# Kernel optimization log

Hardware: AMD Instinct MI355X
Metric: run time of the kernel (lower is better)

## Reference

```python
import jax, jax.numpy as jnp
import numpy as np

VAR_N, LEVELS, NCELLS, PRED_N = 4, 17, 56, 12
D = VAR_N * LEVELS          # 68
FLAT = VAR_N * D            # 272 = ntiles * interm in CrossConnector
T = 4096
DT = 0.1                    # fused-ODE solver step of the LTC cell


def _var_encoder(x, w1, b1, w2, b2, w3, b3, w4, b4, w5, b5):
    # nn.Sequential(Linear, ReLU, Linear, ReLU, Linear, ReLU, Linear, ReLU, Linear)
    h = jax.nn.relu(x @ w1 + b1)
    h = jax.nn.relu(h @ w2 + b2)
    h = jax.nn.relu(h @ w3 + b3)
    h = jax.nn.relu(h @ w4 + b4)
    return h @ w5 + b5


def _run_ltc(seq, wx, wh, b, a, tau, wout, bout):
    def cell(h, u):
        f = jax.nn.sigmoid(u @ wx + h @ wh + b)           # gated synaptic activation
        return (h + DT * f * a) / (1.0 + DT * (1.0 / (tau + 0.5) + f))

    def step_obs(h, u):
        h2 = cell(h, u)
        return h2, h2 @ wout + bout

    hT, vs1 = jax.lax.scan(step_obs, jnp.zeros((NCELLS,), seq.dtype), seq)

    def step_pred(carry, _):
        h, v = carry
        h2 = cell(h, v)
        v2 = h2 @ wout + bout
        return (h2, v2), v2

    _, vs2 = jax.lax.scan(step_pred, (hT, vs1[-1]), None, length=PRED_N)
    return jnp.concatenate([vs1, vs2], axis=0)        # (T+PRED_N, LEVELS)


def setup_inputs() -> dict:
    key = jax.random.key(0)
    ks = iter(jax.random.split(key, 64))
    d = {"x": jax.random.normal(next(ks), (T, D), jnp.float32)}

    def add_ve(prefix, inp, out):
        dims = [(inp, inp), (inp, inp), (inp, out), (out, out), (out, out)]
        for i, (fi, fo) in enumerate(dims, 1):
            d[f"{prefix}w{i}"] = jax.random.normal(next(ks), (fi, fo), jnp.float32) / np.sqrt(fi)
            d[f"{prefix}b{i}"] = jax.random.normal(next(ks), (fo,), jnp.float32) * 0.01

    add_ve("p", D, D)          # preproc  VarEncoder(68,68)
    add_ve("c1", LEVELS, D)    # CrossConnector inner VarEncoder(17,68)
    add_ve("c2", FLAT, D)      # CrossConnector outer VarEncoder(272,68)

    d["ltc_wx"] = jax.random.normal(next(ks), (VAR_N, LEVELS, NCELLS), jnp.float32) / np.sqrt(LEVELS)
    d["ltc_wh"] = jax.random.normal(next(ks), (VAR_N, NCELLS, NCELLS), jnp.float32) / np.sqrt(NCELLS)
    d["ltc_b"] = jax.random.normal(next(ks), (VAR_N, NCELLS), jnp.float32) * 0.01
    d["ltc_a"] = jax.random.normal(next(ks), (VAR_N, NCELLS), jnp.float32)
    d["ltc_tau"] = jax.random.uniform(next(ks), (VAR_N, NCELLS), jnp.float32)
    d["ltc_wout"] = jax.random.normal(next(ks), (VAR_N, NCELLS, LEVELS), jnp.float32) / np.sqrt(NCELLS)
    d["ltc_bout"] = jax.random.normal(next(ks), (VAR_N, LEVELS), jnp.float32) * 0.01
    return d


def reference(x, pw1, pb1, pw2, pb2, pw3, pb3, pw4, pb4, pw5, pb5,
              c1w1, c1b1, c1w2, c1b2, c1w3, c1b3, c1w4, c1b4, c1w5, c1b5,
              c2w1, c2b1, c2w2, c2b2, c2w3, c2b3, c2w4, c2b4, c2w5, c2b5,
              ltc_wx, ltc_wh, ltc_b, ltc_a, ltc_tau, ltc_wout, ltc_bout):
    pre = _var_encoder(x, pw1, pb1, pw2, pb2, pw3, pb3, pw4, pb4, pw5, pb5)   # (T, 68)
    xs = pre.reshape(VAR_N, -1, LEVELS)                                       # (4, T, 17) row-major, as torch.reshape
    vs = jax.vmap(_run_ltc)(xs, ltc_wx, ltc_wh, ltc_b, ltc_a, ltc_tau,
                            ltc_wout, ltc_bout)                               # (4, T+12, 17)
    vs = jnp.transpose(vs, (1, 0, 2))                                         # (T+12, 4, 17)
    y = jax.nn.relu(_var_encoder(vs, c1w1, c1b1, c1w2, c1b2, c1w3, c1b3,
                                 c1w4, c1b4, c1w5, c1b5))                     # (T+12, 4, 68)
    y = y.reshape(y.shape[0], -1)                                             # (T+12, 272)
    return _var_encoder(y, c2w1, c2b1, c2w2, c2b2, c2w3, c2b3,
                        c2w4, c2b4, c2w5, c2b5)                               # (T+12, 68)
```

## Files before the change

kernel.cpp:

```cpp
#include <hip/hip_runtime.h>
#include <hip/hip_bf16.h>
#include <math.h>

#define VAR_N 4
#define LEVELS 17
#define NCELLS 56
#define PRED_N 12
#define TSTEPS 4096
#define TROWS (TSTEPS + PRED_N)
#define DT 0.1f
#define RPB 8
#define LOG2E 1.44269504088896340736f
#define TB 8

static __device__ __forceinline__ float rl(float x, int lane) {
    return __int_as_float(__builtin_amdgcn_readlane(__float_as_int(x), lane));
}
static __device__ __forceinline__ float rcpf(float x) {
    return __builtin_amdgcn_rcpf(x);
}

__global__ void pre_g_kernel(const float* __restrict__ x,
                             const float* __restrict__ w1, const float* __restrict__ b1,
                             const float* __restrict__ w2, const float* __restrict__ b2,
                             const float* __restrict__ w3, const float* __restrict__ b3,
                             const float* __restrict__ w4, const float* __restrict__ b4,
                             const float* __restrict__ w5, const float* __restrict__ b5,
                             const float* __restrict__ wx, const float* __restrict__ bvec,
                             float* __restrict__ g) {
    __shared__ float lds[2 * RPB * 68];
    float* bufA = lds;
    float* bufB = lds + RPB * 68;
    const int r0 = blockIdx.x * RPB;
    const int tid = threadIdx.x;

    for (int idx = tid; idx < RPB * 68; idx += 256)
        bufA[idx] = x[(size_t)r0 * 68 + idx];
    __syncthreads();

    const float* Ws[5] = {w1, w2, w3, w4, w5};
    const float* Bs[5] = {b1, b2, b3, b4, b5};
    for (int L = 0; L < 5; ++L) {
        const float* __restrict__ W = Ws[L];
        const bool act = (L < 4);
        if (tid < 68) {
            const int j = tid;
            float acc[RPB];
            float bj = Bs[L][j];
#pragma unroll
            for (int r = 0; r < RPB; ++r) acc[r] = bj;
            for (int k = 0; k + 4 <= 68; k += 4) {
                float w0v = W[(k + 0) * 68 + j];
                float w1v = W[(k + 1) * 68 + j];
                float w2v = W[(k + 2) * 68 + j];
                float w3v = W[(k + 3) * 68 + j];
#pragma unroll
                for (int r = 0; r < RPB; ++r) {
                    const float4 hx = *(const float4*)(bufA + r * 68 + k);
                    acc[r] = fmaf(hx.x, w0v, fmaf(hx.y, w1v,
                              fmaf(hx.z, w2v, fmaf(hx.w, w3v, acc[r]))));
                }
            }
#pragma unroll
            for (int r = 0; r < RPB; ++r)
                bufB[r * 68 + j] = act ? fmaxf(acc[r], 0.f) : acc[r];
        }
        __syncthreads();
        float* t = bufA; bufA = bufB; bufB = t;
    }

    for (int idx = tid; idx < RPB * 4 * NCELLS; idx += 256) {
        int r = idx / 224;
        int rem = idx - r * 224;
        int q = rem / NCELLS;
        int j = rem - q * NCELLS;
        int gr = r0 + r;
        int v = gr >> 10;
        int trow = ((gr & 1023) << 2) + q;
        const float* arow = bufA + r * 68 + q * LEVELS;
        float acc = bvec[v * NCELLS + j];
#pragma unroll
        for (int l = 0; l < LEVELS; ++l)
            acc = fmaf(arow[l], wx[(v * LEVELS + l) * NCELLS + j], acc);
        g[((size_t)(v * NCELLS + j)) * TSTEPS + trow] = acc * LOG2E;
    }
}

__global__ void __launch_bounds__(64, 1) scan_kernel(
    const float* __restrict__ g, const float* __restrict__ wh,
    const float* __restrict__ a, const float* __restrict__ tau,
    const float* __restrict__ wx, const float* __restrict__ wout,
    const float* __restrict__ bout, const float* __restrict__ b,
    float* __restrict__ H) {
    typedef float v2 __attribute__((ext_vector_type(2)));
    const int v = blockIdx.x;
    const int lane = threadIdx.x;
    const bool active = lane < NCELLS;
    const int j = active ? lane : (NCELLS - 1);
    __shared__ __align__(16) float hbuf[64];

    v2 whp[28];
#pragma unroll
    for (int q = 0; q < 28; ++q) {
        float w0 = active ? wh[((size_t)v * NCELLS + 2 * q + 0) * NCELLS + lane] * LOG2E : 0.f;
        float w1 = active ? wh[((size_t)v * NCELLS + 2 * q + 1) * NCELLS + lane] * LOG2E : 0.f;
        v2 t; t.x = w0; t.y = w1;
        whp[q] = t;
    }
    const float alpha = active ? DT * a[v * NCELLS + lane] : 0.f;
    const float cden = active ? 1.f + DT / (tau[v * NCELLS + lane] + 0.5f) : 1.f;

    const float4* __restrict__ gv4 = (const float4*)(g + ((size_t)v * NCELLS + j) * TSTEPS);
    float* __restrict__ hp = H + (size_t)v * TROWS * NCELLS + lane;

    auto cell = [&](float h, float gcur) -> float {
        hbuf[lane] = h;
        const float4* h4 = (const float4*)hbuf;
        float4 hv[14];
#pragma unroll
        for (int q = 0; q < 14; ++q) hv[q] = h4[q];
        v2 a0 = {0.f, 0.f}, a1 = {0.f, 0.f}, a2 = {0.f, 0.f}, a3 = {0.f, 0.f};
#pragma unroll
        for (int q = 0; q < 7; ++q) {
            float4 hq0 = hv[2 * q];
            float4 hq1 = hv[2 * q + 1];
            v2 p0; p0.x = hq0.x; p0.y = hq0.y;
            v2 p1; p1.x = hq0.z; p1.y = hq0.w;
            v2 p2; p2.x = hq1.x; p2.y = hq1.y;
            v2 p3; p3.x = hq1.z; p3.y = hq1.w;
            a0 = __builtin_elementwise_fma(p0, whp[4 * q + 0], a0);
            a1 = __builtin_elementwise_fma(p1, whp[4 * q + 1], a1);
            a2 = __builtin_elementwise_fma(p2, whp[4 * q + 2], a2);
            a3 = __builtin_elementwise_fma(p3, whp[4 * q + 3], a3);
        }
        v2 s = (a0 + a1) + (a2 + a3);
        float z2 = (gcur + s.x) + s.y;
        float zc = fmaxf(z2, -80.f);
        float e = __builtin_amdgcn_exp2f(-zc);
        float t1 = 1.f + e;
        float num = fmaf(h, t1, alpha);
        float den = fmaf(cden, t1, DT);
        float hn = num * rcpf(den);
        __builtin_amdgcn_sched_group_barrier(0x200, 1, 0);
        __builtin_amdgcn_sched_group_barrier(0x100, 14, 0);
        __builtin_amdgcn_sched_group_barrier(0x002, 40, 0);
        return hn;
    };

    float h = 0.f;
    float4 gq = gv4[0];
    for (int tq = 0; tq < TSTEPS / 4; ++tq) {
        float4 gn = gq;
        if (tq + 1 < TSTEPS / 4) gn = gv4[tq + 1];
        h = cell(h, gq.x); if (active) hp[0 * NCELLS] = h;
        h = cell(h, gq.y); if (active) hp[1 * NCELLS] = h;
        h = cell(h, gq.z); if (active) hp[2 * NCELLS] = h;
        h = cell(h, gq.w); if (active) hp[3 * NCELLS] = h;
        hp += 4 * NCELLS;
        gq = gn;
    }

    float wxcol[LEVELS];
#pragma unroll
    for (int l = 0; l < LEVELS; ++l)
        wxcol[l] = active ? wx[(v * LEVELS + l) * NCELLS + lane] * LOG2E : 0.f;
    float wtc[NCELLS];
#pragma unroll
    for (int jj = 0; jj < NCELLS; ++jj)
        wtc[jj] = (lane < LEVELS) ? wout[((size_t)v * NCELLS + jj) * LEVELS + lane] : 0.f;
    const float bj = active ? b[v * NCELLS + lane] * LOG2E : 0.f;
    const float boutl = (lane < LEVELS) ? bout[v * LEVELS + lane] : 0.f;

    float vv = boutl;
#pragma unroll
    for (int jj = 0; jj < NCELLS; ++jj) vv = fmaf(rl(h, jj), wtc[jj], vv);

    for (int i = 0; i < PRED_N; ++i) {
        float z2 = bj;
#pragma unroll
        for (int l = 0; l < LEVELS; ++l) z2 = fmaf(rl(vv, l), wxcol[l], z2);
#pragma unroll
        for (int k = 0; k < NCELLS; ++k) {
            float wk = (k & 1) ? whp[k >> 1].y : whp[k >> 1].x;
            z2 = fmaf(rl(h, k), wk, z2);
        }
        float zc = fmaxf(z2, -80.f);
        float e = __builtin_amdgcn_exp2f(-zc);
        float t1 = 1.f + e;
        h = fmaf(h, t1, alpha) * rcpf(fmaf(cden, t1, DT));
        if (active) hp[0] = h;
        hp += NCELLS;
        vv = boutl;
#pragma unroll
        for (int jj = 0; jj < NCELLS; ++jj) vv = fmaf(rl(h, jj), wtc[jj], vv);
    }
}

__global__ void __launch_bounds__(256) c1c2_kernel(
    const float* __restrict__ H,
    const float* __restrict__ wout, const float* __restrict__ bout,
    const float* __restrict__ c1w1, const float* __restrict__ c1b1,
    const float* __restrict__ c1w2, const float* __restrict__ c1b2,
    const float* __restrict__ c1w3, const float* __restrict__ c1b3,
    const float* __restrict__ c1w4, const float* __restrict__ c1b4,
    const float* __restrict__ c1w5, const float* __restrict__ c1b5,
    const float* __restrict__ c2w1, const float* __restrict__ c2b1,
    const float* __restrict__ c2w2, const float* __restrict__ c2b2,
    const float* __restrict__ c2w3, const float* __restrict__ c2b3,
    const float* __restrict__ c2w4, const float* __restrict__ c2b4,
    const float* __restrict__ c2w5, const float* __restrict__ c2b5,
    float* __restrict__ out) {
    __shared__ __align__(16) float sH[32 * 56];
    __shared__ __align__(16) float nA[32 * 20];
    __shared__ __align__(16) float nB[32 * 20];
    __shared__ __align__(16) float bY[TB * 272];
    __shared__ __align__(16) float bZ[TB * 272];
    const int t0 = blockIdx.x * TB;
    const int tid = threadIdx.x;

    for (int idx = tid; idx < 32 * 56; idx += 256) {
        int row = idx / 56, jj = idx - (idx / 56) * 56;
        int tq = row >> 2, v = row & 3;
        int t = t0 + tq;
        sH[idx] = (t < TROWS) ? H[((size_t)v * TROWS + t) * 56 + jj] : 0.f;
    }
    __syncthreads();

    if (tid < 136) {
        int l = tid % 17;
        int rg = tid / 17;
        int v = rg & 3, th = rg >> 2;
        float acc[4];
        float bl = bout[v * 17 + l];
#pragma unroll
        for (int q = 0; q < 4; ++q) acc[q] = bl;
        for (int k = 0; k < 56; k += 4) {
            float w0 = wout[(v * 56 + k + 0) * 17 + l];
            float w1 = wout[(v * 56 + k + 1) * 17 + l];
            float w2 = wout[(v * 56 + k + 2) * 17 + l];
            float w3 = wout[(v * 56 + k + 3) * 17 + l];
#pragma unroll
            for (int q = 0; q < 4; ++q) {
                const float4 hx = *(const float4*)(sH + ((th * 4 + q) * 4 + v) * 56 + k);
                acc[q] = fmaf(hx.x, w0, fmaf(hx.y, w1, fmaf(hx.z, w2, fmaf(hx.w, w3, acc[q]))));
            }
        }
#pragma unroll
        for (int q = 0; q < 4; ++q) nA[((th * 4 + q) * 4 + v) * 20 + l] = acc[q];
    }
    __syncthreads();

#pragma unroll
    for (int LL = 0; LL < 2; ++LL) {
        const float* W = LL ? c1w2 : c1w1;
        const float* B = LL ? c1b2 : c1b1;
        const float* in = LL ? nB : nA;
        float* ob = LL ? nA : nB;
        if (tid < 136) {
            int l = tid % 17;
            int rg = tid / 17;
            float acc[4];
            float bl = B[l];
#pragma unroll
            for (int q = 0; q < 4; ++q) acc[q] = bl;
            for (int k = 0; k + 4 <= 17; k += 4) {
                float w0 = W[(k + 0) * 17 + l], w1 = W[(k + 1) * 17 + l];
                float w2 = W[(k + 2) * 17 + l], w3 = W[(k + 3) * 17 + l];
#pragma unroll
                for (int q = 0; q < 4; ++q) {
                    const float4 hx = *(const float4*)(in + (rg * 4 + q) * 20 + k);
                    acc[q] = fmaf(hx.x, w0, fmaf(hx.y, w1, fmaf(hx.z, w2, fmaf(hx.w, w3, acc[q]))));
                }
            }
            float w16 = W[16 * 17 + l];
#pragma unroll
            for (int q = 0; q < 4; ++q)
                ob[(rg * 4 + q) * 20 + l] = fmaxf(fmaf(in[(rg * 4 + q) * 20 + 16], w16, acc[q]), 0.f);
        }
        __syncthreads();
    }

    if (tid < 136) {
        int j = tid % 68;
        int rg = tid / 68;
        float acc[16];
        float bj = c1b3[j];
#pragma unroll
        for (int r = 0; r < 16; ++r) acc[r] = bj;
        for (int k = 0; k + 4 <= 17; k += 4) {
            float w0 = c1w3[(k + 0) * 68 + j], w1 = c1w3[(k + 1) * 68 + j];
            float w2 = c1w3[(k + 2) * 68 + j], w3 = c1w3[(k + 3) * 68 + j];
#pragma unroll
            for (int r = 0; r < 16; ++r) {
                const float4 hx = *(const float4*)(nA + (rg * 16 + r) * 20 + k);
                acc[r] = fmaf(hx.x, w0, fmaf(hx.y, w1, fmaf(hx.z, w2, fmaf(hx.w, w3, acc[r]))));
            }
        }
        float w16 = c1w3[16 * 68 + j];
#pragma unroll
        for (int r = 0; r < 16; ++r)
            bY[(rg * 16 + r) * 68 + j] = fmaxf(fmaf(nA[(rg * 16 + r) * 20 + 16], w16, acc[r]), 0.f);
    }
    __syncthreads();

#pragma unroll
    for (int LL = 0; LL < 2; ++LL) {
        const float* W = LL ? c1w5 : c1w4;
        const float* B = LL ? c1b5 : c1b4;
        const float* in = LL ? bZ : bY;
        float* ob = LL ? bY : bZ;
        if (tid < 136) {
            int j = tid % 68;
            int rg = tid / 68;
            float acc[16];
            float bj = B[j];
#pragma unroll
            for (int r = 0; r < 16; ++r) acc[r] = bj;
            for (int k = 0; k < 68; k += 4) {
                float w0 = W[(k + 0) * 68 + j], w1 = W[(k + 1) * 68 + j];
                float w2 = W[(k + 2) * 68 + j], w3 = W[(k + 3) * 68 + j];
#pragma unroll
                for (int r = 0; r < 16; ++r) {
                    const float4 hx = *(const float4*)(in + (rg * 16 + r) * 68 + k);
                    acc[r] = fmaf(hx.x, w0, fmaf(hx.y, w1, fmaf(hx.z, w2, fmaf(hx.w, w3, acc[r]))));
                }
            }
#pragma unroll
            for (int r = 0; r < 16; ++r)
                ob[(rg * 16 + r) * 68 + j] = fmaxf(acc[r], 0.f);
        }
        __syncthreads();
    }

#pragma unroll
    for (int LL = 0; LL < 2; ++LL) {
        const float* W = LL ? c2w2 : c2w1;
        const float* B = LL ? c2b2 : c2b1;
        const float* in = LL ? bZ : bY;
        float* ob = LL ? bY : bZ;
        if (tid < 136) {
            int j = 2 * tid;
            float acc0[TB], acc1[TB];
            float b0 = B[j], b1 = B[j + 1];
#pragma unroll
            for (int r = 0; r < TB; ++r) { acc0[r] = b0; acc1[r] = b1; }
            for (int k = 0; k < 272; k += 4) {
                float2 w0 = *(const float2*)(W + (size_t)(k + 0) * 272 + j);
                float2 w1 = *(const float2*)(W + (size_t)(k + 1) * 272 + j);
                float2 w2 = *(const float2*)(W + (size_t)(k + 2) * 272 + j);
                float2 w3 = *(const float2*)(W + (size_t)(k + 3) * 272 + j);
#pragma unroll
                for (int r = 0; r < TB; ++r) {
                    const float4 hx = *(const float4*)(in + r * 272 + k);
                    acc0[r] = fmaf(hx.x, w0.x, fmaf(hx.y, w1.x, fmaf(hx.z, w2.x, fmaf(hx.w, w3.x, acc0[r]))));
                    acc1[r] = fmaf(hx.x, w0.y, fmaf(hx.y, w1.y, fmaf(hx.z, w2.y, fmaf(hx.w, w3.y, acc1[r]))));
                }
            }
#pragma unroll
            for (int r = 0; r < TB; ++r) {
                ob[r * 272 + j] = fmaxf(acc0[r], 0.f);
                ob[r * 272 + j + 1] = fmaxf(acc1[r], 0.f);
            }
        }
        __syncthreads();
    }

    if (tid < 136) {
        int j = tid % 68;
        int rg = tid / 68;
        float acc[4];
        float bj = c2b3[j];
#pragma unroll
        for (int r = 0; r < 4; ++r) acc[r] = bj;
        for (int k = 0; k < 272; k += 4) {
            float w0 = c2w3[(size_t)(k + 0) * 68 + j], w1 = c2w3[(size_t)(k + 1) * 68 + j];
            float w2 = c2w3[(size_t)(k + 2) * 68 + j], w3 = c2w3[(size_t)(k + 3) * 68 + j];
#pragma unroll
            for (int r = 0; r < 4; ++r) {
                const float4 hx = *(const float4*)(bY + (rg * 4 + r) * 272 + k);
                acc[r] = fmaf(hx.x, w0, fmaf(hx.y, w1, fmaf(hx.z, w2, fmaf(hx.w, w3, acc[r]))));
            }
        }
#pragma unroll
        for (int r = 0; r < 4; ++r)
            bZ[(rg * 4 + r) * 68 + j] = fmaxf(acc[r], 0.f);
    }
    __syncthreads();

#pragma unroll
    for (int LL = 0; LL < 2; ++LL) {
        const float* W = LL ? c2w5 : c2w4;
        const float* B = LL ? c2b5 : c2b4;
        const float* in = LL ? bY : bZ;
        float* ob = LL ? bZ : bY;
        const bool act = (LL == 0);
        if (tid < 136) {
            int j = tid % 68;
            int rg = tid / 68;
            float acc[4];
            float bj = B[j];
#pragma unroll
            for (int r = 0; r < 4; ++r) acc[r] = bj;
            for (int k = 0; k < 68; k += 4) {
                float w0 = W[(k + 0) * 68 + j], w1 = W[(k + 1) * 68 + j];
                float w2 = W[(k + 2) * 68 + j], w3 = W[(k + 3) * 68 + j];
#pragma unroll
                for (int r = 0; r < 4; ++r) {
                    const float4 hx = *(const float4*)(in + (rg * 4 + r) * 68 + k);
                    acc[r] = fmaf(hx.x, w0, fmaf(hx.y, w1, fmaf(hx.z, w2, fmaf(hx.w, w3, acc[r]))));
                }
            }
#pragma unroll
            for (int r = 0; r < 4; ++r)
                ob[(rg * 4 + r) * 68 + j] = act ? fmaxf(acc[r], 0.f) : acc[r];
        }
        __syncthreads();
    }

    for (int idx = tid; idx < TB * 68; idx += 256) {
        int r = idx / 68, c = idx - (idx / 68) * 68;
        int t = t0 + r;
        if (t < TROWS) out[(size_t)t * 68 + c] = bZ[r * 68 + c];
    }
}

extern "C" void kernel_launch(void* const* d_in, const int* in_sizes, int n_in,
                              void* d_out, int out_size, void* d_ws, size_t ws_size,
                              hipStream_t stream) {
    const float* x = (const float*)d_in[0];
    const float* pw[5] = {(const float*)d_in[1], (const float*)d_in[3], (const float*)d_in[5],
                          (const float*)d_in[7], (const float*)d_in[9]};
    const float* pb[5] = {(const float*)d_in[2], (const float*)d_in[4], (const float*)d_in[6],
                          (const float*)d_in[8], (const float*)d_in[10]};
    const float* c1w[5] = {(const float*)d_in[11], (const float*)d_in[13], (const float*)d_in[15],
                           (const float*)d_in[17], (const float*)d_in[19]};
    const float* c1b[5] = {(const float*)d_in[12], (const float*)d_in[14], (const float*)d_in[16],
                           (const float*)d_in[18], (const float*)d_in[20]};
    const float* c2w[5] = {(const float*)d_in[21], (const float*)d_in[23], (const float*)d_in[25],
                           (const float*)d_in[27], (const float*)d_in[29]};
    const float* c2b[5] = {(const float*)d_in[22], (const float*)d_in[24], (const float*)d_in[26],
                           (const float*)d_in[28], (const float*)d_in[30]};
    const float* ltc_wx = (const float*)d_in[31];
    const float* ltc_wh = (const float*)d_in[32];
    const float* ltc_b = (const float*)d_in[33];
    const float* ltc_a = (const float*)d_in[34];
    const float* ltc_tau = (const float*)d_in[35];
    const float* ltc_wout = (const float*)d_in[36];
    const float* ltc_bout = (const float*)d_in[37];

    float* ws = (float*)d_ws;
    float* g = ws;
    float* H = g + 917504;
    float* out = (float*)d_out;

    pre_g_kernel<<<TSTEPS / RPB, 256, 0, stream>>>(
        x, pw[0], pb[0], pw[1], pb[1], pw[2], pb[2], pw[3], pb[3], pw[4], pb[4],
        ltc_wx, ltc_b, g);

    scan_kernel<<<VAR_N, 64, 0, stream>>>(g, ltc_wh, ltc_a, ltc_tau, ltc_wx,
                                          ltc_wout, ltc_bout, ltc_b, H);

    c1c2_kernel<<<(TROWS + TB - 1) / TB, 256, 0, stream>>>(
        H, ltc_wout, ltc_bout,
        c1w[0], c1b[0], c1w[1], c1b[1], c1w[2], c1b[2], c1w[3], c1b[3], c1w[4], c1b[4],
        c2w[0], c2b[0], c2w[1], c2b[1], c2w[2], c2b[2], c2w[3], c2b[3], c2w[4], c2b[4],
        out);
}
```

Measured before the change: 1.047 ms.

## Fuse three kernels into persistent kernel with producer-consumer flag pipelining

Replaces the three separate launches (preprocessing, sequential LTC scan, cross-connector MLP) with one persistent kernel. Four blocks run the scans, and the rest first compute g tiles, then consume H tiles as the scan publishes its progress through atomic counters. Each scan starts once its variable's g slice is complete. This lets the cross-connector work overlap the long serial scan and removes launch gaps, at the cost of spin-wait synchronisation, an extra memset, and a dependence on all blocks being co-resident.

Measured after the change: 1.166 ms. +11.4%, slower.

```diff
diff --git a/kernel.cpp b/kernel.cpp
--- a/kernel.cpp
+++ b/kernel.cpp
@@ -12,6 +12,9 @@
 #define RPB 8
 #define LOG2E 1.44269504088896340736f
 #define TB 8
+#define NCONS 252
+#define NGT 512
+#define NCT 514
 
 static __device__ __forceinline__ float rl(float x, int lane) {
     return __int_as_float(__builtin_amdgcn_readlane(__float_as_int(x), lane));
@@ -20,19 +23,17 @@
     return __builtin_amdgcn_rcpf(x);
 }
 
-__global__ void pre_g_kernel(const float* __restrict__ x,
-                             const float* __restrict__ w1, const float* __restrict__ b1,
-                             const float* __restrict__ w2, const float* __restrict__ b2,
-                             const float* __restrict__ w3, const float* __restrict__ b3,
-                             const float* __restrict__ w4, const float* __restrict__ b4,
-                             const float* __restrict__ w5, const float* __restrict__ b5,
-                             const float* __restrict__ wx, const float* __restrict__ bvec,
-                             float* __restrict__ g) {
-    __shared__ float lds[2 * RPB * 68];
-    float* bufA = lds;
-    float* bufB = lds + RPB * 68;
-    const int r0 = blockIdx.x * RPB;
-    const int tid = threadIdx.x;
+static __device__ void preg_tile(int r0, int tid, float* smem,
+    const float* __restrict__ x,
+    const float* __restrict__ w1, const float* __restrict__ b1,
+    const float* __restrict__ w2, const float* __restrict__ b2,
+    const float* __restrict__ w3, const float* __restrict__ b3,
+    const float* __restrict__ w4, const float* __restrict__ b4,
+    const float* __restrict__ w5, const float* __restrict__ b5,
+    const float* __restrict__ wx, const float* __restrict__ bvec,
+    float* __restrict__ g) {
+    float* bufA = smem;
+    float* bufB = smem + RPB * 68;
 
     for (int idx = tid; idx < RPB * 68; idx += 256)
         bufA[idx] = x[(size_t)r0 * 68 + idx];
@@ -86,117 +87,7 @@
     }
 }
 
-__global__ void __launch_bounds__(64, 1) scan_kernel(
-    const float* __restrict__ g, const float* __restrict__ wh,
-    const float* __restrict__ a, const float* __restrict__ tau,
-    const float* __restrict__ wx, const float* __restrict__ wout,
-    const float* __restrict__ bout, const float* __restrict__ b,
-    float* __restrict__ H) {
-    typedef float v2 __attribute__((ext_vector_type(2)));
-    const int v = blockIdx.x;
-    const int lane = threadIdx.x;
-    const bool active = lane < NCELLS;
-    const int j = active ? lane : (NCELLS - 1);
-    __shared__ __align__(16) float hbuf[64];
-
-    v2 whp[28];
-#pragma unroll
-    for (int q = 0; q < 28; ++q) {
-        float w0 = active ? wh[((size_t)v * NCELLS + 2 * q + 0) * NCELLS + lane] * LOG2E : 0.f;
-        float w1 = active ? wh[((size_t)v * NCELLS + 2 * q + 1) * NCELLS + lane] * LOG2E : 0.f;
-        v2 t; t.x = w0; t.y = w1;
-        whp[q] = t;
-    }
-    const float alpha = active ? DT * a[v * NCELLS + lane] : 0.f;
-    const float cden = active ? 1.f + DT / (tau[v * NCELLS + lane] + 0.5f) : 1.f;
-
-    const float4* __restrict__ gv4 = (const float4*)(g + ((size_t)v * NCELLS + j) * TSTEPS);
-    float* __restrict__ hp = H + (size_t)v * TROWS * NCELLS + lane;
-
-    auto cell = [&](float h, float gcur) -> float {
-        hbuf[lane] = h;
-        const float4* h4 = (const float4*)hbuf;
-        float4 hv[14];
-#pragma unroll
-        for (int q = 0; q < 14; ++q) hv[q] = h4[q];
-        v2 a0 = {0.f, 0.f}, a1 = {0.f, 0.f}, a2 = {0.f, 0.f}, a3 = {0.f, 0.f};
-#pragma unroll
-        for (int q = 0; q < 7; ++q) {
-            float4 hq0 = hv[2 * q];
-            float4 hq1 = hv[2 * q + 1];
-            v2 p0; p0.x = hq0.x; p0.y = hq0.y;
-            v2 p1; p1.x = hq0.z; p1.y = hq0.w;
-            v2 p2; p2.x = hq1.x; p2.y = hq1.y;
-            v2 p3; p3.x = hq1.z; p3.y = hq1.w;
-            a0 = __builtin_elementwise_fma(p0, whp[4 * q + 0], a0);
-            a1 = __builtin_elementwise_fma(p1, whp[4 * q + 1], a1);
-            a2 = __builtin_elementwise_fma(p2, whp[4 * q + 2], a2);
-            a3 = __builtin_elementwise_fma(p3, whp[4 * q + 3], a3);
-        }
-        v2 s = (a0 + a1) + (a2 + a3);
-        float z2 = (gcur + s.x) + s.y;
-        float zc = fmaxf(z2, -80.f);
-        float e = __builtin_amdgcn_exp2f(-zc);
-        float t1 = 1.f + e;
-        float num = fmaf(h, t1, alpha);
-        float den = fmaf(cden, t1, DT);
-        float hn = num * rcpf(den);
-        __builtin_amdgcn_sched_group_barrier(0x200, 1, 0);
-        __builtin_amdgcn_sched_group_barrier(0x100, 14, 0);
-        __builtin_amdgcn_sched_group_barrier(0x002, 40, 0);
-        return hn;
-    };
-
-    float h = 0.f;
-    float4 gq = gv4[0];
-    for (int tq = 0; tq < TSTEPS / 4; ++tq) {
-        float4 gn = gq;
-        if (tq + 1 < TSTEPS / 4) gn = gv4[tq + 1];
-        h = cell(h, gq.x); if (active) hp[0 * NCELLS] = h;
-        h = cell(h, gq.y); if (active) hp[1 * NCELLS] = h;
-        h = cell(h, gq.z); if (active) hp[2 * NCELLS] = h;
-        h = cell(h, gq.w); if (active) hp[3 * NCELLS] = h;
-        hp += 4 * NCELLS;
-        gq = gn;
-    }
-
-    float wxcol[LEVELS];
-#pragma unroll
-    for (int l = 0; l < LEVELS; ++l)
-        wxcol[l] = active ? wx[(v * LEVELS + l) * NCELLS + lane] * LOG2E : 0.f;
-    float wtc[NCELLS];
-#pragma unroll
-    for (int jj = 0; jj < NCELLS; ++jj)
-        wtc[jj] = (lane < LEVELS) ? wout[((size_t)v * NCELLS + jj) * LEVELS + lane] : 0.f;
-    const float bj = active ? b[v * NCELLS + lane] * LOG2E : 0.f;
-    const float boutl = (lane < LEVELS) ? bout[v * LEVELS + lane] : 0.f;
-
-    float vv = boutl;
-#pragma unroll
-    for (int jj = 0; jj < NCELLS; ++jj) vv = fmaf(rl(h, jj), wtc[jj], vv);
-
-    for (int i = 0; i < PRED_N; ++i) {
-        float z2 = bj;
-#pragma unroll
-        for (int l = 0; l < LEVELS; ++l) z2 = fmaf(rl(vv, l), wxcol[l], z2);
-#pragma unroll
-        for (int k = 0; k < NCELLS; ++k) {
-            float wk = (k & 1) ? whp[k >> 1].y : whp[k >> 1].x;
-            z2 = fmaf(rl(h, k), wk, z2);
-        }
-        float zc = fmaxf(z2, -80.f);
-        float e = __builtin_amdgcn_exp2f(-zc);
-        float t1 = 1.f + e;
-        h = fmaf(h, t1, alpha) * rcpf(fmaf(cden, t1, DT));
-        if (active) hp[0] = h;
-        hp += NCELLS;
-        vv = boutl;
-#pragma unroll
-        for (int jj = 0; jj < NCELLS; ++jj) vv = fmaf(rl(h, jj), wtc[jj], vv);
-    }
-}
-
-__global__ void __launch_bounds__(256) c1c2_kernel(
+static __device__ void c1c2_tile(int t0, int tid, float* smem,
     const float* __restrict__ H,
     const float* __restrict__ wout, const float* __restrict__ bout,
     const float* __restrict__ c1w1, const float* __restrict__ c1b1,
@@ -210,13 +101,11 @@
     const float* __restrict__ c2w4, const float* __restrict__ c2b4,
     const float* __restrict__ c2w5, const float* __restrict__ c2b5,
     float* __restrict__ out) {
-    __shared__ __align__(16) float sH[32 * 56];
-    __shared__ __align__(16) float nA[32 * 20];
-    __shared__ __align__(16) float nB[32 * 20];
-    __shared__ __align__(16) float bY[TB * 272];
-    __shared__ __align__(16) float bZ[TB * 272];
-    const int t0 = blockIdx.x * TB;
-    const int tid = threadIdx.x;
+    float* sH = smem;
+    float* nA = smem + 1792;
+    float* nB = smem + 2432;
+    float* bY = smem + 3072;
+    float* bZ = smem + 5248;
 
     for (int idx = tid; idx < 32 * 56; idx += 256) {
         int row = idx / 56, jj = idx - (idx / 56) * 56;
@@ -421,6 +310,195 @@
         int r = idx / 68, c = idx - (idx / 68) * 68;
         int t = t0 + r;
         if (t < TROWS) out[(size_t)t * 68 + c] = bZ[r * 68 + c];
+    }
+}
+
+__global__ void __launch_bounds__(256, 1) fused_kernel(
+    const float* __restrict__ x,
+    const float* __restrict__ pw1, const float* __restrict__ pb1,
+    const float* __restrict__ pw2, const float* __restrict__ pb2,
+    const float* __restrict__ pw3, const float* __restrict__ pb3,
+    const float* __restrict__ pw4, const float* __restrict__ pb4,
+    const float* __restrict__ pw5, const float* __restrict__ pb5,
+    const float* __restrict__ c1w1, const float* __restrict__ c1b1,
+    const float* __restrict__ c1w2, const float* __restrict__ c1b2,
+    const float* __restrict__ c1w3, const float* __restrict__ c1b3,
+    const float* __restrict__ c1w4, const float* __restrict__ c1b4,
+    const float* __restrict__ c1w5, const float* __restrict__ c1b5,
+    const float* __restrict__ c2w1, const float* __restrict__ c2b1,
+    const float* __restrict__ c2w2, const float* __restrict__ c2b2,
+    const float* __restrict__ c2w3, const float* __restrict__ c2b3,
+    const float* __restrict__ c2w4, const float* __restrict__ c2b4,
+    const float* __restrict__ c2w5, const float* __restrict__ c2b5,
+    const float* __restrict__ wx, const float* __restrict__ wh,
+    const float* __restrict__ bvec, const float* __restrict__ av,
+    const float* __restrict__ tauv, const float* __restrict__ wout,
+    const float* __restrict__ boutv,
+    float* __restrict__ g, float* __restrict__ H,
+    int* gdone, int* prog, float* __restrict__ out) {
+    __shared__ __align__(16) float smem[7424];
+    const int bid = blockIdx.x;
+    const int tid = threadIdx.x;
+
+    if (bid < VAR_N) {
+        if (tid >= 64) return;
+        typedef float v2 __attribute__((ext_vector_type(2)));
+        const int v = bid;
+        const int lane = tid;
+        const bool active = lane < NCELLS;
+        const int j = active ? lane : (NCELLS - 1);
+        float* hbuf = smem;
+
+        v2 whp[28];
+#pragma unroll
+        for (int q = 0; q < 28; ++q) {
+            float w0 = active ? wh[((size_t)v * NCELLS + 2 * q + 0) * NCELLS + lane] * LOG2E : 0.f;
+            float w1 = active ? wh[((size_t)v * NCELLS + 2 * q + 1) * NCELLS + lane] * LOG2E : 0.f;
+            v2 t; t.x = w0; t.y = w1;
+            whp[q] = t;
+        }
+        const float alpha = active ? DT * av[v * NCELLS + lane] : 0.f;
+        const float cden = active ? 1.f + DT / (tauv[v * NCELLS + lane] + 0.5f) : 1.f;
+
+        if (lane == 0) {
+            while (__hip_atomic_load(&gdone[v], __ATOMIC_RELAXED, __HIP_MEMORY_SCOPE_AGENT) < 128)
+                __builtin_amdgcn_s_sleep(16);
+            (void)__hip_atomic_load(&gdone[v], __ATOMIC_ACQUIRE, __HIP_MEMORY_SCOPE_AGENT);
+        }
+
+        const float4* __restrict__ gv4 = (const float4*)(g + ((size_t)v * NCELLS + j) * TSTEPS);
+        float* __restrict__ hp = H + (size_t)v * TROWS * NCELLS + lane;
+
+        auto cell = [&](float h, float gcur) -> float {
+            hbuf[lane] = h;
+            const float4* h4 = (const float4*)hbuf;
+            float4 hv[14];
+#pragma unroll
+            for (int q = 0; q < 14; ++q) hv[q] = h4[q];
+            v2 a0 = {0.f, 0.f}, a1 = {0.f, 0.f}, a2 = {0.f, 0.f}, a3 = {0.f, 0.f};
+#pragma unroll
+            for (int q = 0; q < 7; ++q) {
+                float4 hq0 = hv[2 * q];
+                float4 hq1 = hv[2 * q + 1];
+                v2 p0; p0.x = hq0.x; p0.y = hq0.y;
+                v2 p1; p1.x = hq0.z; p1.y = hq0.w;
+                v2 p2; p2.x = hq1.x; p2.y = hq1.y;
+                v2 p3; p3.x = hq1.z; p3.y = hq1.w;
+                a0 = __builtin_elementwise_fma(p0, whp[4 * q + 0], a0);
+                a1 = __builtin_elementwise_fma(p1, whp[4 * q + 1], a1);
+                a2 = __builtin_elementwise_fma(p2, whp[4 * q + 2], a2);
+                a3 = __builtin_elementwise_fma(p3, whp[4 * q + 3], a3);
+            }
+            v2 s = (a0 + a1) + (a2 + a3);
+            float z2 = (gcur + s.x) + s.y;
+            float zc = fmaxf(z2, -80.f);
+            float e = __builtin_amdgcn_exp2f(-zc);
+            float t1 = 1.f + e;
+            float num = fmaf(h, t1, alpha);
+            float den = fmaf(cden, t1, DT);
+            float hn = num * rcpf(den);
+            __builtin_amdgcn_sched_group_barrier(0x200, 1, 0);
+            __builtin_amdgcn_sched_group_barrier(0x100, 14, 0);
+            __builtin_amdgcn_sched_group_barrier(0x002, 40, 0);
+            return hn;
+        };
+
+        float h = 0.f;
+        float4 gq = gv4[0];
+        for (int tq = 0; tq < TSTEPS / 4; ++tq) {
+            float4 gn = gq;
+            if (tq + 1 < TSTEPS / 4) gn = gv4[tq + 1];
+            h = cell(h, gq.x); if (active) hp[0 * NCELLS] = h;
+            h = cell(h, gq.y); if (active) hp[1 * NCELLS] = h;
+            h = cell(h, gq.z); if (active) hp[2 * NCELLS] = h;
+            h = cell(h, gq.w); if (active) hp[3 * NCELLS] = h;
+            hp += 4 * NCELLS;
+            gq = gn;
+            if ((tq & 31) == 31) {
+                __threadfence();
+                if (lane == 0)
+                    __hip_atomic_store(&prog[v], 4 * (tq + 1), __ATOMIC_RELEASE,
+                                       __HIP_MEMORY_SCOPE_AGENT);
+            }
+        }
+
+        float wxcol[LEVELS];
+#pragma unroll
+        for (int l = 0; l < LEVELS; ++l)
+            wxcol[l] = active ? wx[(v * LEVELS + l) * NCELLS + lane] * LOG2E : 0.f;
+        float wtc[NCELLS];
+#pragma unroll
+        for (int jj = 0; jj < NCELLS; ++jj)
+            wtc[jj] = (lane < LEVELS) ? wout[((size_t)v * NCELLS + jj) * LEVELS + lane] : 0.f;
+        const float bj = active ? bvec[v * NCELLS + lane] * LOG2E : 0.f;
+        const float boutl = (lane < LEVELS) ? boutv[v * LEVELS + lane] : 0.f;
+
+        float vv = boutl;
+#pragma unroll
+        for (int jj = 0; jj < NCELLS; ++jj) vv = fmaf(rl(h, jj), wtc[jj], vv);
+
+        for (int i = 0; i < PRED_N; ++i) {
+            float z2 = bj;
+#pragma unroll
+            for (int l = 0; l < LEVELS; ++l) z2 = fmaf(rl(vv, l), wxcol[l], z2);
+#pragma unroll
+            for (int k = 0; k < NCELLS; ++k) {
+                float wk = (k & 1) ? whp[k >> 1].y : whp[k >> 1].x;
+                z2 = fmaf(rl(h, k), wk, z2);
+            }
+            float zc = fmaxf(z2, -80.f);
+            float e = __builtin_amdgcn_exp2f(-zc);
+            float t1 = 1.f + e;
+            h = fmaf(h, t1, alpha) * rcpf(fmaf(cden, t1, DT));
+            if (active) hp[0] = h;
+            hp += NCELLS;
+            vv = boutl;
+#pragma unroll
+            for (int jj = 0; jj < NCELLS; ++jj) vv = fmaf(rl(h, jj), wtc[jj], vv);
+        }
+        __threadfence();
+        if (lane == 0)
+            __hip_atomic_store(&prog[v], TROWS, __ATOMIC_RELEASE, __HIP_MEMORY_SCOPE_AGENT);
+        return;
+    }
+
+    const int cb = bid - VAR_N;
+
+    for (int gt = cb; gt < NGT; gt += NCONS) {
+        preg_tile(gt * RPB, tid, smem, x,
+                  pw1, pb1, pw2, pb2, pw3, pb3, pw4, pb4, pw5, pb5,
+                  wx, bvec, g);
+        __threadfence();
+        __syncthreads();
+        if (tid == 0) {
+            int vt = (gt * RPB) >> 10;
+            __hip_atomic_fetch_add(&gdone[vt], 1, __ATOMIC_RELEASE, __HIP_MEMORY_SCOPE_AGENT);
+        }
+        __syncthreads();
+    }
+
+    for (int tile = cb; tile < NCT; tile += NCONS) {
+        int t0 = tile * TB;
+        int need = t0 + TB;
+        if (need > TROWS) need = TROWS;
+        if (tid == 0) {
+            for (;;) {
+                int m0 = __hip_atomic_load(&prog[0], __ATOMIC_RELAXED, __HIP_MEMORY_SCOPE_AGENT);
+                int m1 = __hip_atomic_load(&prog[1], __ATOMIC_RELAXED, __HIP_MEMORY_SCOPE_AGENT);
+                int m2 = __hip_atomic_load(&prog[2], __ATOMIC_RELAXED, __HIP_MEMORY_SCOPE_AGENT);
+                int m3 = __hip_atomic_load(&prog[3], __ATOMIC_RELAXED, __HIP_MEMORY_SCOPE_AGENT);
+                int mn = min(min(m0, m1), min(m2, m3));
+                if (mn >= need) break;
+                __builtin_amdgcn_s_sleep(32);
+            }
+            (void)__hip_atomic_load(&prog[0], __ATOMIC_ACQUIRE, __HIP_MEMORY_SCOPE_AGENT);
+        }
+        __syncthreads();
+        c1c2_tile(t0, tid, smem, H, wout, boutv,
+                  c1w1, c1b1, c1w2, c1b2, c1w3, c1b3, c1w4, c1b4, c1w5, c1b5,
+                  c2w1, c2b1, c2w2, c2b2, c2w3, c2b3, c2w4, c2b4, c2w5, c2b5,
+                  out);
+        __syncthreads();
     }
 }
 
@@ -451,18 +529,18 @@
     float* ws = (float*)d_ws;
     float* g = ws;
     float* H = g + 917504;
+    int* ctrl = (int*)(H + 920192);
+    int* gdone = ctrl;
+    int* prog = ctrl + 4;
     float* out = (float*)d_out;
 
-    pre_g_kernel<<<TSTEPS / RPB, 256, 0, stream>>>(
-        x, pw[0], pb[0], pw[1], pb[1], pw[2], pb[2], pw[3], pb[3], pw[4], pb[4],
-        ltc_wx, ltc_b, g);
-
-    scan_kernel<<<VAR_N, 64, 0, stream>>>(g, ltc_wh, ltc_a, ltc_tau, ltc_wx,
-                                          ltc_wout, ltc_bout, ltc_b, H);
-
-    c1c2_kernel<<<(TROWS + TB - 1) / TB, 256, 0, stream>>>(
-        H, ltc_wout, ltc_bout,
+    hipMemsetAsync(ctrl, 0, 8 * sizeof(int), stream);
+
+    fused_kernel<<<VAR_N + NCONS, 256, 0, stream>>>(
+        x,
+        pw[0], pb[0], pw[1], pb[1], pw[2], pb[2], pw[3], pb[3], pw[4], pb[4],
         c1w[0], c1b[0], c1w[1], c1b[1], c1w[2], c1b[2], c1w[3], c1b[3], c1w[4], c1b[4],
         c2w[0], c2b[0], c2w[1], c2b[1], c2w[2], c2b[2], c2w[3], c2b[3], c2w[4], c2b[4],
-        out);
+        ltc_wx, ltc_wh, ltc_b, ltc_a, ltc_tau, ltc_wout, ltc_bout,
+        g, H, gdone, prog, out);
 }
```

## Replace LDS broadcast in LTC scan matvec with DPP wave rotation

Applied to the files above, without the earlier changes.

The recurrent h·Wh product in the scan kernel no longer writes h to shared memory and reads it back as float4s. Instead each lane keeps a rotated copy of its weight column in 64 registers. It then rotates h around the wavefront with a DPP wave_rol move, accumulating 64 FMAs into four partial sums. This removes the per-step LDS store and load latency from the serial recurrence. In exchange it puts a dependent chain of 64 DPP moves plus 64 scalar FMAs in place of about 28 packed FMAs, and drops the explicit scheduling barriers.

New measurement: 1.855 ms. +77.3%, slower.

```diff
diff --git a/kernel.cpp b/kernel.cpp
--- a/kernel.cpp
+++ b/kernel.cpp
@@ -18,6 +18,9 @@
 }
 static __device__ __forceinline__ float rcpf(float x) {
     return __builtin_amdgcn_rcpf(x);
+}
+static __device__ __forceinline__ float rotl1(float x) {
+    return __int_as_float(__builtin_amdgcn_mov_dpp(__float_as_int(x), 0x134, 0xF, 0xF, false));
 }
 
 __global__ void pre_g_kernel(const float* __restrict__ x,
@@ -92,20 +95,18 @@
     const float* __restrict__ wx, const float* __restrict__ wout,
     const float* __restrict__ bout, const float* __restrict__ b,
     float* __restrict__ H) {
-    typedef float v2 __attribute__((ext_vector_type(2)));
     const int v = blockIdx.x;
     const int lane = threadIdx.x;
     const bool active = lane < NCELLS;
     const int j = active ? lane : (NCELLS - 1);
-    __shared__ __align__(16) float hbuf[64];
-
-    v2 whp[28];
-#pragma unroll
-    for (int q = 0; q < 28; ++q) {
-        float w0 = active ? wh[((size_t)v * NCELLS + 2 * q + 0) * NCELLS + lane] * LOG2E : 0.f;
-        float w1 = active ? wh[((size_t)v * NCELLS + 2 * q + 1) * NCELLS + lane] * LOG2E : 0.f;
-        v2 t; t.x = w0; t.y = w1;
-        whp[q] = t;
+
+    float wrot[64];
+#pragma unroll
+    for (int i = 0; i < 64; ++i) {
+        int k = (lane + i) & 63;
+        wrot[i] = (active && k < NCELLS)
+                      ? wh[((size_t)v * NCELLS + k) * NCELLS + lane] * LOG2E
+                      : 0.f;
     }
     const float alpha = active ? DT * a[v * NCELLS + lane] : 0.f;
     const float cden = active ? 1.f + DT / (tau[v * NCELLS + lane] + 0.5f) : 1.f;
@@ -114,37 +115,24 @@
     float* __restrict__ hp = H + (size_t)v * TROWS * NCELLS + lane;
 
     auto cell = [&](float h, float gcur) -> float {
-        hbuf[lane] = h;
-        const float4* h4 = (const float4*)hbuf;
-        float4 hv[14];
-#pragma unroll
-        for (int q = 0; q < 14; ++q) hv[q] = h4[q];
-        v2 a0 = {0.f, 0.f}, a1 = {0.f, 0.f}, a2 = {0.f, 0.f}, a3 = {0.f, 0.f};
-#pragma unroll
-        for (int q = 0; q < 7; ++q) {
-            float4 hq0 = hv[2 * q];
-            float4 hq1 = hv[2 * q + 1];
-            v2 p0; p0.x = hq0.x; p0.y = hq0.y;
-            v2 p1; p1.x = hq0.z; p1.y = hq0.w;
-            v2 p2; p2.x = hq1.x; p2.y = hq1.y;
-            v2 p3; p3.x = hq1.z; p3.y = hq1.w;
-            a0 = __builtin_elementwise_fma(p0, whp[4 * q + 0], a0);
-            a1 = __builtin_elementwise_fma(p1, whp[4 * q + 1], a1);
-            a2 = __builtin_elementwise_fma(p2, whp[4 * q + 2], a2);
-            a3 = __builtin_elementwise_fma(p3, whp[4 * q + 3], a3);
-        }
-        v2 s = (a0 + a1) + (a2 + a3);
-        float z2 = (gcur + s.x) + s.y;
+        float hr = h;
+        float z0 = gcur, z1 = 0.f, z2a = 0.f, z3 = 0.f;
+#pragma unroll
+        for (int i = 0; i < 64; ++i) {
+            float w = wrot[i];
+            if ((i & 3) == 0) z0 = fmaf(hr, w, z0);
+            else if ((i & 3) == 1) z1 = fmaf(hr, w, z1);
+            else if ((i & 3) == 2) z2a = fmaf(hr, w, z2a);
+            else z3 = fmaf(hr, w, z3);
+            if (i < 63) hr = rotl1(hr);
+        }
+        float z2 = (z0 + z1) + (z2a + z3);
         float zc = fmaxf(z2, -80.f);
         float e = __builtin_amdgcn_exp2f(-zc);
         float t1 = 1.f + e;
         float num = fmaf(h, t1, alpha);
         float den = fmaf(cden, t1, DT);
-        float hn = num * rcpf(den);
-        __builtin_amdgcn_sched_group_barrier(0x200, 1, 0);
-        __builtin_amdgcn_sched_group_barrier(0x100, 14, 0);
-        __builtin_amdgcn_sched_group_barrier(0x002, 40, 0);
-        return hn;
+        return num * rcpf(den);
     };
 
     float h = 0.f;
@@ -179,10 +167,11 @@
         float z2 = bj;
 #pragma unroll
         for (int l = 0; l < LEVELS; ++l) z2 = fmaf(rl(vv, l), wxcol[l], z2);
-#pragma unroll
-        for (int k = 0; k < NCELLS; ++k) {
-            float wk = (k & 1) ? whp[k >> 1].y : whp[k >> 1].x;
-            z2 = fmaf(rl(h, k), wk, z2);
+        float hr = h;
+#pragma unroll
+        for (int q = 0; q < 64; ++q) {
+            z2 = fmaf(hr, wrot[q], z2);
+            if (q < 63) hr = rotl1(hr);
         }
         float zc = fmaxf(z2, -80.f);
         float e = __builtin_amdgcn_exp2f(-zc);
```
